# Kernel optimization log

Measured on AMD Instinct MI355X. Metric: run time of the kernel, lower is better.

Reference implementation:

```python
import jax, jax.numpy as jnp
import numpy as np

QUALITY = 75

Y_TABLE = np.array([
    [16, 11, 10, 16, 24, 40, 51, 61],
    [12, 12, 14, 19, 26, 58, 60, 55],
    [14, 13, 16, 24, 40, 57, 69, 56],
    [14, 17, 22, 29, 51, 87, 80, 62],
    [18, 22, 37, 56, 68, 109, 103, 77],
    [24, 35, 55, 64, 81, 104, 113, 92],
    [49, 64, 78, 87, 103, 121, 120, 101],
    [72, 92, 95, 98, 112, 100, 103, 99]], dtype=np.float32)

C_TABLE = np.array([
    [17, 18, 24, 47, 99, 99, 99, 99],
    [18, 21, 26, 66, 99, 99, 99, 99],
    [24, 26, 56, 99, 99, 99, 99, 99],
    [47, 66, 99, 99, 99, 99, 99, 99],
    [99, 99, 99, 99, 99, 99, 99, 99],
    [99, 99, 99, 99, 99, 99, 99, 99],
    [99, 99, 99, 99, 99, 99, 99, 99],
    [99, 99, 99, 99, 99, 99, 99, 99]], dtype=np.float32)

def _dct_mat():
    # Orthonormal 8-point DCT-II matrix D: coef = D @ block @ D.T
    xg = np.arange(8, dtype=np.float64)
    ug = np.arange(8, dtype=np.float64)
    D = 0.5 * np.cos((2.0 * xg[None, :] + 1.0) * ug[:, None] * np.pi / 16.0)
    D[0, :] *= 1.0 / np.sqrt(2.0)
    return jnp.asarray(D, dtype=jnp.float32)

D8 = _dct_mat()

def _blockify(ch):
    # [B,H,W] -> [B, H//8, W//8, 8, 8]
    B, H, W = ch.shape
    return ch.reshape(B, H // 8, 8, W // 8, 8).transpose(0, 1, 3, 2, 4)

def _deblockify(blk):
    # [B, hb, wb, 8, 8] -> [B, hb*8, wb*8]
    B, hb, wb, _, _ = blk.shape
    return blk.transpose(0, 1, 3, 2, 4).reshape(B, hb * 8, wb * 8)

def _channel_jpeg(ch, table, factor):
    # ch: [B,H,W] in 0..255 -> quantize/dequantize in DCT domain
    q = table * factor  # [8,8]
    blk = _blockify(ch - 128.0)                                   # [B,hb,wb,8,8]
    coef = jnp.einsum('bhwxy,ux,vy->bhwuv', blk, D8, D8)           # 8x8 DCT
    coef = jnp.round(coef / q) * q                                 # quantize + dequantize
    rec = jnp.einsum('bhwuv,ux,vy->bhwxy', coef, D8, D8) + 128.0   # IDCT
    return _deblockify(rec)

def jpeg_compress(img, quality):
    # img: [B,3,H,W] in [0,1]
    if quality < 50:
        factor = 5000.0 / quality
    else:
        factor = 200.0 - 2.0 * quality
    factor = factor / 100.0
    x = img * 255.0
    r, g, b = x[:, 0], x[:, 1], x[:, 2]
    y = 0.299 * r + 0.587 * g + 0.114 * b
    cb = -0.168736 * r - 0.331264 * g + 0.5 * b + 128.0
    cr = 0.5 * r - 0.418688 * g - 0.081312 * b + 128.0
    # 4:2:0 chroma subsampling via 2x2 average pooling
    B, H, W = cb.shape
    cb_s = cb.reshape(B, H // 2, 2, W // 2, 2).mean(axis=(2, 4))
    cr_s = cr.reshape(B, H // 2, 2, W // 2, 2).mean(axis=(2, 4))
    y_r = _channel_jpeg(y, jnp.asarray(Y_TABLE), factor)
    cb_r = _channel_jpeg(cb_s, jnp.asarray(C_TABLE), factor)
    cr_r = _channel_jpeg(cr_s, jnp.asarray(C_TABLE), factor)
    # nearest-neighbor chroma upsampling
    cb_u = jnp.repeat(jnp.repeat(cb_r, 2, axis=1), 2, axis=2)
    cr_u = jnp.repeat(jnp.repeat(cr_r, 2, axis=1), 2, axis=2)
    cbm = cb_u - 128.0
    crm = cr_u - 128.0
    r2 = y_r + 1.402 * crm
    g2 = y_r - 0.344136 * cbm - 0.714136 * crm
    b2 = y_r + 1.772 * cbm
    out = jnp.stack([r2, g2, b2], axis=1)
    return jnp.clip(out, 0.0, 255.0) / 255.0


def setup_inputs() -> dict:
    key = jax.random.key(0)
    x = jax.random.uniform(key, (16, 3, 512, 512), dtype=jnp.float32)
    return {"x": x}


def reference(x):
    img_clip = jnp.clip(x, 0.0, 1.0)
    img_jpeg = jpeg_compress(img_clip, QUALITY)
    img_gap = jax.lax.stop_gradient(img_jpeg - x)
    return x + img_gap
```

## Files before the change

### kernel.cpp

```cpp
#include <hip/hip_runtime.h>
#include <math.h>

#define CH_STRIDE (512 * 512)

static constexpr float DMc[8][8] = {
  { 0.35355339059327373f, 0.35355339059327373f, 0.35355339059327373f, 0.35355339059327373f,
    0.35355339059327373f, 0.35355339059327373f, 0.35355339059327373f, 0.35355339059327373f},
  { 0.49039264020161522f, 0.41573480615127262f, 0.27778511650980111f, 0.09754516100806413f,
   -0.09754516100806413f,-0.27778511650980111f,-0.41573480615127262f,-0.49039264020161522f},
  { 0.46193976625564337f, 0.19134171618254489f,-0.19134171618254489f,-0.46193976625564337f,
   -0.46193976625564337f,-0.19134171618254489f, 0.19134171618254489f, 0.46193976625564337f},
  { 0.41573480615127262f,-0.09754516100806413f,-0.49039264020161522f,-0.27778511650980111f,
    0.27778511650980111f, 0.49039264020161522f, 0.09754516100806413f,-0.41573480615127262f},
  { 0.35355339059327373f,-0.35355339059327373f,-0.35355339059327373f, 0.35355339059327373f,
    0.35355339059327373f,-0.35355339059327373f,-0.35355339059327373f, 0.35355339059327373f},
  { 0.27778511650980111f,-0.49039264020161522f, 0.09754516100806413f, 0.41573480615127262f,
   -0.41573480615127262f,-0.09754516100806413f, 0.49039264020161522f,-0.27778511650980111f},
  { 0.19134171618254489f,-0.46193976625564337f, 0.46193976625564337f,-0.19134171618254489f,
   -0.19134171618254489f, 0.46193976625564337f,-0.46193976625564337f, 0.19134171618254489f},
  { 0.09754516100806413f,-0.27778511650980111f, 0.41573480615127262f,-0.49039264020161522f,
    0.49039264020161522f,-0.41573480615127262f, 0.27778511650980111f,-0.09754516100806413f},
};

static constexpr float QTABc[128] = {
   8.0f,  5.5f,  5.0f,  8.0f, 12.0f, 20.0f, 25.5f, 30.5f,
   6.0f,  6.0f,  7.0f,  9.5f, 13.0f, 29.0f, 30.0f, 27.5f,
   7.0f,  6.5f,  8.0f, 12.0f, 20.0f, 28.5f, 34.5f, 28.0f,
   7.0f,  8.5f, 11.0f, 14.5f, 25.5f, 43.5f, 40.0f, 31.0f,
   9.0f, 11.0f, 18.5f, 28.0f, 34.0f, 54.5f, 51.5f, 38.5f,
  12.0f, 17.5f, 27.5f, 32.0f, 40.5f, 52.0f, 56.5f, 46.0f,
  24.5f, 32.0f, 39.0f, 43.5f, 51.5f, 60.5f, 60.0f, 50.5f,
  36.0f, 46.0f, 47.5f, 49.0f, 56.0f, 50.0f, 51.5f, 49.5f,

   8.5f,  9.0f, 12.0f, 23.5f, 49.5f, 49.5f, 49.5f, 49.5f,
   9.0f, 10.5f, 13.0f, 33.0f, 49.5f, 49.5f, 49.5f, 49.5f,
  12.0f, 13.0f, 28.0f, 49.5f, 49.5f, 49.5f, 49.5f, 49.5f,
  23.5f, 33.0f, 49.5f, 49.5f, 49.5f, 49.5f, 49.5f, 49.5f,
  49.5f, 49.5f, 49.5f, 49.5f, 49.5f, 49.5f, 49.5f, 49.5f,
  49.5f, 49.5f, 49.5f, 49.5f, 49.5f, 49.5f, 49.5f, 49.5f,
  49.5f, 49.5f, 49.5f, 49.5f, 49.5f, 49.5f, 49.5f, 49.5f,
  49.5f, 49.5f, 49.5f, 49.5f, 49.5f, 49.5f, 49.5f, 49.5f,
};

__device__ __forceinline__ float fm(float a, float b) { return __fmul_rn(a, b); }
__device__ __forceinline__ float fa(float a, float b) { return __fadd_rn(a, b); }
__device__ __forceinline__ float fs(float a, float b) { return __fsub_rn(a, b); }
__device__ __forceinline__ float fd(float a, float b) { return __fdiv_rn(a, b); }

__global__ __launch_bounds__(256, 4)
void jpeg_kernel(const float* __restrict__ x, float* __restrict__ out) {
  const int tid = threadIdx.x;
  const int q  = blockIdx.x;
  const int b  = q >> 8;
  const int qq = q & 255;
  const int row0 = (qq >> 4) << 5;
  const int col0 = (qq & 15) << 5;

  __shared__ __align__(16) float Ys[32][36];
  __shared__ __align__(16) float CbBlk[16][20];
  __shared__ __align__(16) float CrBlk[16][20];
  __shared__ __align__(16) float Cq[24][8][9];
  __shared__ __align__(16) float CbR[16][20];
  __shared__ __align__(16) float CrR[16][20];

  const int pr = tid >> 3;
  const int pc = (tid & 7) << 2;
  const size_t ibase = ((((size_t)b * 3) * 512 + (size_t)(row0 + pr)) * 512) + (size_t)(col0 + pc);

  {
    float4 rv = *(const float4*)(x + ibase);
    float4 gv = *(const float4*)(x + ibase + CH_STRIDE);
    float4 bv = *(const float4*)(x + ibase + 2 * CH_STRIDE);
    float xr[4] = {rv.x, rv.y, rv.z, rv.w};
    float xg[4] = {gv.x, gv.y, gv.z, gv.w};
    float xb[4] = {bv.x, bv.y, bv.z, bv.w};
    float yo[4], cbv[4], crv[4];
#pragma unroll
    for (int i = 0; i < 4; ++i) {
      float r  = fm(fminf(fmaxf(xr[i], 0.0f), 1.0f), 255.0f);
      float g  = fm(fminf(fmaxf(xg[i], 0.0f), 1.0f), 255.0f);
      float bb = fm(fminf(fmaxf(xb[i], 0.0f), 1.0f), 255.0f);
      float y  = fa(fa(fm(0.299f, r), fm(0.587f, g)), fm(0.114f, bb));
      yo[i]  = fs(y, 128.0f);
      cbv[i] = fa(fa(fs(fm(-0.168736f, r), fm(0.331264f, g)), fm(0.5f, bb)), 128.0f);
      crv[i] = fa(fs(fs(fm(0.5f, r), fm(0.418688f, g)), fm(0.081312f, bb)), 128.0f);
    }
    *(float4*)&Ys[pr][pc] = make_float4(yo[0], yo[1], yo[2], yo[3]);

    float cbh0 = fa(cbv[0], cbv[1]), cbh1 = fa(cbv[2], cbv[3]);
    float crh0 = fa(crv[0], crv[1]), crh1 = fa(crv[2], crv[3]);
    float pcb0 = __shfl_xor(cbh0, 8, 64);
    float pcb1 = __shfl_xor(cbh1, 8, 64);
    float pcr0 = __shfl_xor(crh0, 8, 64);
    float pcr1 = __shfl_xor(crh1, 8, 64);
    if (((tid >> 3) & 1) == 0) {
      const int ii = pr >> 1, jc = pc >> 1;
      CbBlk[ii][jc]     = fs(fm(fa(cbh0, pcb0), 0.25f), 128.0f);
      CbBlk[ii][jc + 1] = fs(fm(fa(cbh1, pcb1), 0.25f), 128.0f);
      CrBlk[ii][jc]     = fs(fm(fa(crh0, pcr0), 0.25f), 128.0f);
      CrBlk[ii][jc + 1] = fs(fm(fa(crh1, pcr1), 0.25f), 128.0f);
    }
  }
  __syncthreads();

  const int  blk = tid >> 3;
  const int  j   = tid & 7;
  const bool act = tid < 192;
  const bool isY = blk < 16;
  const float* src  = nullptr;
  float*       wdst = nullptr;
  int ld = 36;
  const float* qr = QTABc + j * 8;
  if (act) {
    if (isY) {
      const int by = blk >> 2, bx = blk & 3;
      src = &Ys[by * 8][bx * 8];  wdst = &Ys[by * 8 + j][bx * 8];  ld = 36;
    } else if (blk < 20) {
      const int c = blk - 16, cy = c >> 1, cx = c & 1;
      src = &CbBlk[cy * 8][cx * 8];  wdst = &CbR[cy * 8 + j][cx * 8];  ld = 20;  qr += 64;
    } else {
      const int c = blk - 20, cy = c >> 1, cx = c & 1;
      src = &CrBlk[cy * 8][cx * 8];  wdst = &CrR[cy * 8 + j][cx * 8];  ld = 20;  qr += 64;
    }
  }

  if (act) {
    float dj[8];
#pragma unroll
    for (int xx = 0; xx < 8; ++xx) dj[xx] = DMc[j][xx];
    float s[8][4];
#pragma unroll
    for (int v = 0; v < 8; ++v) { s[v][0] = 0.0f; s[v][1] = 0.0f; s[v][2] = 0.0f; s[v][3] = 0.0f; }
    const float* srow = src;
#pragma unroll
    for (int xx = 0; xx < 8; ++xx) {
      float4 aq = *(const float4*)(srow);
      float4 bq = *(const float4*)(srow + 4);
      srow += ld;
      float t0r[8] = { fm(aq.x, dj[xx]), fm(aq.y, dj[xx]), fm(aq.z, dj[xx]), fm(aq.w, dj[xx]),
                       fm(bq.x, dj[xx]), fm(bq.y, dj[xx]), fm(bq.z, dj[xx]), fm(bq.w, dj[xx]) };
#pragma unroll
      for (int v = 0; v < 8; ++v) {
        s[v][0] = fa(s[v][0], fm(t0r[0], DMc[v][0]));
        s[v][1] = fa(s[v][1], fm(t0r[1], DMc[v][1]));
        s[v][2] = fa(s[v][2], fm(t0r[2], DMc[v][2]));
        s[v][3] = fa(s[v][3], fm(t0r[3], DMc[v][3]));
        s[v][0] = fa(s[v][0], fm(t0r[4], DMc[v][4]));
        s[v][1] = fa(s[v][1], fm(t0r[5], DMc[v][5]));
        s[v][2] = fa(s[v][2], fm(t0r[6], DMc[v][6]));
        s[v][3] = fa(s[v][3], fm(t0r[7], DMc[v][7]));
      }
    }
    float* cq = &Cq[blk][j][0];
#pragma unroll
    for (int v = 0; v < 8; ++v) {
      float coef = fa(fa(s[v][0], s[v][1]), fa(s[v][2], s[v][3]));
      float qv = qr[v];
      cq[v] = fm(rintf(fd(coef, qv)), qv);
    }
  }
  __syncthreads();

  if (act) {
    float acc[8];
#pragma unroll
    for (int yy = 0; yy < 8; ++yy) acc[yy] = 0.0f;
    const float* cqb = &Cq[blk][0][0];
#pragma unroll
    for (int u = 0; u < 8; ++u) {
      float du = DMc[u][j];
      float t2r[8];
#pragma unroll
      for (int v = 0; v < 8; ++v) t2r[v] = fm(cqb[u * 9 + v], du);
#pragma unroll
      for (int yy = 0; yy < 8; ++yy) {
#pragma unroll
        for (int v = 0; v < 8; ++v)
          acc[yy] = fa(acc[yy], fm(t2r[v], DMc[v][yy]));
      }
    }
    float r0[8];
#pragma unroll
    for (int yy = 0; yy < 8; ++yy) {
      float rec = fa(acc[yy], 128.0f);
      r0[yy] = isY ? rec : fs(rec, 128.0f);
    }
    *(float4*)(wdst)     = make_float4(r0[0], r0[1], r0[2], r0[3]);
    *(float4*)(wdst + 4) = make_float4(r0[4], r0[5], r0[6], r0[7]);
  }
  __syncthreads();

  {
    float4 rv = *(const float4*)(x + ibase);
    float4 gv = *(const float4*)(x + ibase + CH_STRIDE);
    float4 bv = *(const float4*)(x + ibase + 2 * CH_STRIDE);
    float xr[4] = {rv.x, rv.y, rv.z, rv.w};
    float xg[4] = {gv.x, gv.y, gv.z, gv.w};
    float xb[4] = {bv.x, bv.y, bv.z, bv.w};
    float ro[4], go[4], bo[4];
    const int hr = pr >> 1;
#pragma unroll
    for (int i = 0; i < 4; ++i) {
      float y_r = Ys[pr][pc + i];
      float cbm = CbR[hr][(pc + i) >> 1];
      float crm = CrR[hr][(pc + i) >> 1];
      float r2 = fa(y_r, fm(1.402f, crm));
      float g2 = fs(fs(y_r, fm(0.344136f, cbm)), fm(0.714136f, crm));
      float b2 = fa(y_r, fm(1.772f, cbm));
      float jr = fd(fminf(fmaxf(r2, 0.0f), 255.0f), 255.0f);
      float jg = fd(fminf(fmaxf(g2, 0.0f), 255.0f), 255.0f);
      float jb = fd(fminf(fmaxf(b2, 0.0f), 255.0f), 255.0f);
      ro[i] = fa(xr[i], fs(jr, xr[i]));
      go[i] = fa(xg[i], fs(jg, xg[i]));
      bo[i] = fa(xb[i], fs(jb, xb[i]));
    }
    *(float4*)(out + ibase)                 = make_float4(ro[0], ro[1], ro[2], ro[3]);
    *(float4*)(out + ibase + CH_STRIDE)     = make_float4(go[0], go[1], go[2], go[3]);
    *(float4*)(out + ibase + 2 * CH_STRIDE) = make_float4(bo[0], bo[1], bo[2], bo[3]);
  }
}

extern "C" void kernel_launch(void* const* d_in, const int* in_sizes, int n_in,
                              void* d_out, int out_size, void* d_ws, size_t ws_size,
                              hipStream_t stream) {
  const float* x = (const float*)d_in[0];
  float* out = (float*)d_out;
  jpeg_kernel<<<dim3(4096), dim3(256), 0, stream>>>(x, out);
}
```

Measured before the change: 116.3 us.

## Drop idle wave, reuse chroma buffers, replace mid barrier with LDS waitcnt

The block shrinks from 256 to 192 threads so that no wave sits idle during the DCT and IDCT phases. The first 64 threads now do a second quad during load/convert and writeback. The separate reconstructed-chroma LDS buffers are merged into the input chroma buffers, which reduces shared-memory use and allows more resident blocks (launch bounds 192, 8). The barrier between the DCT and IDCT phases becomes an s_waitcnt. This relies on each 8-thread group living in one wavefront, at the cost of an uneven per-wave workload in the global-memory phases.

```diff
diff --git a/kernel.cpp b/kernel.cpp
--- a/kernel.cpp
+++ b/kernel.cpp
@@ -47,7 +47,7 @@
 __device__ __forceinline__ float fs(float a, float b) { return __fsub_rn(a, b); }
 __device__ __forceinline__ float fd(float a, float b) { return __fdiv_rn(a, b); }
 
-__global__ __launch_bounds__(256, 4)
+__global__ __launch_bounds__(192, 8)
 void jpeg_kernel(const float* __restrict__ x, float* __restrict__ out) {
   const int tid = threadIdx.x;
   const int q  = blockIdx.x;
@@ -57,20 +57,17 @@
   const int col0 = (qq & 15) << 5;
 
   __shared__ __align__(16) float Ys[32][36];
-  __shared__ __align__(16) float CbBlk[16][20];
-  __shared__ __align__(16) float CrBlk[16][20];
+  __shared__ __align__(16) float Cb[16][20];
+  __shared__ __align__(16) float Cr[16][20];
   __shared__ __align__(16) float Cq[24][8][9];
-  __shared__ __align__(16) float CbR[16][20];
-  __shared__ __align__(16) float CrR[16][20];
-
-  const int pr = tid >> 3;
-  const int pc = (tid & 7) << 2;
-  const size_t ibase = ((((size_t)b * 3) * 512 + (size_t)(row0 + pr)) * 512) + (size_t)(col0 + pc);
-
-  {
-    float4 rv = *(const float4*)(x + ibase);
-    float4 gv = *(const float4*)(x + ibase + CH_STRIDE);
-    float4 bv = *(const float4*)(x + ibase + 2 * CH_STRIDE);
+
+  auto stage1 = [&](int qd) {
+    const int pr = qd >> 3;
+    const int pc = (qd & 7) << 2;
+    const size_t ib = ((((size_t)b * 3) * 512 + (size_t)(row0 + pr)) * 512) + (size_t)(col0 + pc);
+    float4 rv = *(const float4*)(x + ib);
+    float4 gv = *(const float4*)(x + ib + CH_STRIDE);
+    float4 bv = *(const float4*)(x + ib + 2 * CH_STRIDE);
     float xr[4] = {rv.x, rv.y, rv.z, rv.w};
     float xg[4] = {gv.x, gv.y, gv.z, gv.w};
     float xb[4] = {bv.x, bv.y, bv.z, bv.w};
@@ -93,38 +90,37 @@
     float pcb1 = __shfl_xor(cbh1, 8, 64);
     float pcr0 = __shfl_xor(crh0, 8, 64);
     float pcr1 = __shfl_xor(crh1, 8, 64);
-    if (((tid >> 3) & 1) == 0) {
+    if (((qd >> 3) & 1) == 0) {
       const int ii = pr >> 1, jc = pc >> 1;
-      CbBlk[ii][jc]     = fs(fm(fa(cbh0, pcb0), 0.25f), 128.0f);
-      CbBlk[ii][jc + 1] = fs(fm(fa(cbh1, pcb1), 0.25f), 128.0f);
-      CrBlk[ii][jc]     = fs(fm(fa(crh0, pcr0), 0.25f), 128.0f);
-      CrBlk[ii][jc + 1] = fs(fm(fa(crh1, pcr1), 0.25f), 128.0f);
-    }
-  }
+      Cb[ii][jc]     = fs(fm(fa(cbh0, pcb0), 0.25f), 128.0f);
+      Cb[ii][jc + 1] = fs(fm(fa(cbh1, pcb1), 0.25f), 128.0f);
+      Cr[ii][jc]     = fs(fm(fa(crh0, pcr0), 0.25f), 128.0f);
+      Cr[ii][jc + 1] = fs(fm(fa(crh1, pcr1), 0.25f), 128.0f);
+    }
+  };
+  stage1(tid);
+  if (tid < 64) stage1(192 + tid);
   __syncthreads();
 
   const int  blk = tid >> 3;
   const int  j   = tid & 7;
-  const bool act = tid < 192;
   const bool isY = blk < 16;
-  const float* src  = nullptr;
-  float*       wdst = nullptr;
-  int ld = 36;
+  const float* src;
+  float*       wdst;
+  int ld;
   const float* qr = QTABc + j * 8;
-  if (act) {
-    if (isY) {
-      const int by = blk >> 2, bx = blk & 3;
-      src = &Ys[by * 8][bx * 8];  wdst = &Ys[by * 8 + j][bx * 8];  ld = 36;
-    } else if (blk < 20) {
-      const int c = blk - 16, cy = c >> 1, cx = c & 1;
-      src = &CbBlk[cy * 8][cx * 8];  wdst = &CbR[cy * 8 + j][cx * 8];  ld = 20;  qr += 64;
-    } else {
-      const int c = blk - 20, cy = c >> 1, cx = c & 1;
-      src = &CrBlk[cy * 8][cx * 8];  wdst = &CrR[cy * 8 + j][cx * 8];  ld = 20;  qr += 64;
-    }
+  if (isY) {
+    const int by = blk >> 2, bx = blk & 3;
+    src = &Ys[by * 8][bx * 8];  wdst = &Ys[by * 8 + j][bx * 8];  ld = 36;
+  } else if (blk < 20) {
+    const int c = blk - 16, cy = c >> 1, cx = c & 1;
+    src = &Cb[cy * 8][cx * 8];  wdst = &Cb[cy * 8 + j][cx * 8];  ld = 20;  qr += 64;
+  } else {
+    const int c = blk - 20, cy = c >> 1, cx = c & 1;
+    src = &Cr[cy * 8][cx * 8];  wdst = &Cr[cy * 8 + j][cx * 8];  ld = 20;  qr += 64;
   }
 
-  if (act) {
+  {
     float dj[8];
 #pragma unroll
     for (int xx = 0; xx < 8; ++xx) dj[xx] = DMc[j][xx];
@@ -159,9 +155,10 @@
       cq[v] = fm(rintf(fd(coef, qv)), qv);
     }
   }
-  __syncthreads();
-
-  if (act) {
+
+  asm volatile("s_waitcnt lgkmcnt(0)" ::: "memory");
+
+  {
     float acc[8];
 #pragma unroll
     for (int yy = 0; yy < 8; ++yy) acc[yy] = 0.0f;
@@ -190,10 +187,13 @@
   }
   __syncthreads();
 
-  {
-    float4 rv = *(const float4*)(x + ibase);
-    float4 gv = *(const float4*)(x + ibase + CH_STRIDE);
-    float4 bv = *(const float4*)(x + ibase + 2 * CH_STRIDE);
+  auto stage5 = [&](int qd) {
+    const int pr = qd >> 3;
+    const int pc = (qd & 7) << 2;
+    const size_t ib = ((((size_t)b * 3) * 512 + (size_t)(row0 + pr)) * 512) + (size_t)(col0 + pc);
+    float4 rv = *(const float4*)(x + ib);
+    float4 gv = *(const float4*)(x + ib + CH_STRIDE);
+    float4 bv = *(const float4*)(x + ib + 2 * CH_STRIDE);
     float xr[4] = {rv.x, rv.y, rv.z, rv.w};
     float xg[4] = {gv.x, gv.y, gv.z, gv.w};
     float xb[4] = {bv.x, bv.y, bv.z, bv.w};
@@ -202,8 +202,8 @@
 #pragma unroll
     for (int i = 0; i < 4; ++i) {
       float y_r = Ys[pr][pc + i];
-      float cbm = CbR[hr][(pc + i) >> 1];
-      float crm = CrR[hr][(pc + i) >> 1];
+      float cbm = Cb[hr][(pc + i) >> 1];
+      float crm = Cr[hr][(pc + i) >> 1];
       float r2 = fa(y_r, fm(1.402f, crm));
       float g2 = fs(fs(y_r, fm(0.344136f, cbm)), fm(0.714136f, crm));
       float b2 = fa(y_r, fm(1.772f, cbm));
@@ -214,10 +214,12 @@
       go[i] = fa(xg[i], fs(jg, xg[i]));
       bo[i] = fa(xb[i], fs(jb, xb[i]));
     }
-    *(float4*)(out + ibase)                 = make_float4(ro[0], ro[1], ro[2], ro[3]);
-    *(float4*)(out + ibase + CH_STRIDE)     = make_float4(go[0], go[1], go[2], go[3]);
-    *(float4*)(out + ibase + 2 * CH_STRIDE) = make_float4(bo[0], bo[1], bo[2], bo[3]);
-  }
+    *(float4*)(out + ib)                 = make_float4(ro[0], ro[1], ro[2], ro[3]);
+    *(float4*)(out + ib + CH_STRIDE)     = make_float4(go[0], go[1], go[2], go[3]);
+    *(float4*)(out + ib + 2 * CH_STRIDE) = make_float4(bo[0], bo[1], bo[2], bo[3]);
+  };
+  stage5(tid);
+  if (tid < 64) stage5(192 + tid);
 }
 
 extern "C" void kernel_launch(void* const* d_in, const int* in_sizes, int n_in,
@@ -225,5 +227,5 @@
                               hipStream_t stream) {
   const float* x = (const float*)d_in[0];
   float* out = (float*)d_out;
-  jpeg_kernel<<<dim3(4096), dim3(256), 0, stream>>>(x, out);
+  jpeg_kernel<<<dim3(4096), dim3(192), 0, stream>>>(x, out);
 }
```

Result: slower. 187.6 us (+61.3%).
